# Kernel optimization log

Hardware: AMD Instinct MI355X
Metric: run time of the kernel (lower is better)

Reference implementation:

```python
import jax, jax.numpy as jnp
import numpy as np

NUM_RADII, NUM_THETA = 3, 16
RADIUS = 40.0
DT = 0.1
RELU_SHIFT = 0.2
B, N, NB, T_ENC, OTHER_CH = 4, 512, 512, 16, 3


def _rot_mats():
    # bin-center angles of the num_theta angular bins
    t = (jnp.arange(NUM_THETA, dtype=jnp.float32) + 0.5) * (2.0 * jnp.pi / NUM_THETA) - jnp.pi
    c, s = jnp.cos(t), jnp.sin(t)
    return jnp.stack([jnp.stack([c, -s], -1), jnp.stack([s, c], -1)], -2)  # [T,2,2]


def _steer_kernel(W):
    # W: [R,T,O,I,2,2]; equivariant steering K[r,t] = R(theta_t) W[r,t] R(theta_t)^T
    Rm = _rot_mats()
    K = jnp.einsum('tab,rtoibc,tdc->rtoiad', Rm, W, Rm)
    return K.reshape(NUM_RADII * NUM_THETA, W.shape[2], W.shape[3], 2, 2)  # [K,O,I,2,2]


def _equi_conv(src_pos, qry_pos, feats, mask, W):
    # src_pos [B,S,2], qry_pos [B,Q,2], feats [B,S,I,2] vector features, mask [B,Q,S]
    rel = src_pos[:, None, :, :] - qry_pos[:, :, None, :]          # [B,Q,S,2]
    d2 = jnp.sum(rel * rel, -1)
    dist = jnp.sqrt(d2 + 1e-9)
    theta = jnp.arctan2(rel[..., 1], rel[..., 0])
    rb = jnp.clip((dist / RADIUS * NUM_RADII).astype(jnp.int32), 0, NUM_RADII - 1)
    tb = jnp.mod(jnp.floor((theta + jnp.pi) / (2.0 * jnp.pi) * NUM_THETA).astype(jnp.int32), NUM_THETA)
    kidx = rb * NUM_THETA + tb                                     # [B,Q,S] polar bin id
    win = jnp.maximum(1.0 - d2 / (RADIUS * RADIUS), 0.0) ** 3      # smooth radial window
    w = win * mask
    H = jax.nn.one_hot(kidx, NUM_RADII * NUM_THETA, dtype=feats.dtype) * w[..., None]  # [B,Q,S,K]
    M = jnp.einsum('bqsk,bsiv->bqkiv', H, feats)                   # bin-accumulated neighbor features
    K = _steer_kernel(W)
    return jnp.einsum('bqkiv,koiuv->bqou', M, K)                   # [B,Q,O,2]


def _equi_linear(f, A, Bm):
    # rotation-equivariant linear on vector channels: (a*I + b*J) per (out,in)
    Jf = jnp.stack([-f[..., 1], f[..., 0]], -1)
    return jnp.einsum('oi,bniv->bnov', A, f) + jnp.einsum('oi,bniv->bnov', Bm, Jf)


def _forward(p0_enc, v0_enc, p0, v0, a, other_feats, box, box_feats, fluid_mask, box_mask,
             W_cf, W_co, A_df, B_df, layer_params):
    # update_pos_vel
    v1 = v0 + DT * a
    p1 = p0 + DT * (v0 + v1) * 0.5
    # forward(): feats = cat(other_feats, v0_enc) on channel dim -2
    feats = jnp.concatenate([other_feats, v0_enc], -2)
    # compute_correction
    fluid_feats = jnp.concatenate([v1[:, :, None, :], feats], -2)  # [B,N,20,2]
    out_conv_fluid = _equi_conv(p1, p1, fluid_feats, fluid_mask, W_cf)
    out_dense_fluid = _equi_linear(fluid_feats, A_df, B_df)
    out_conv_obst = _equi_conv(box, p1, box_feats[:, :, None, :], box_mask, W_co)
    output = jnp.concatenate([out_conv_obst, out_conv_fluid, out_dense_fluid], -2)  # [B,N,48,2]
    for (Wc, Ad, Bd) in layer_params:
        mags = (jnp.sum(output * output, -1) + 1e-6)[..., None]
        in_feats = output / mags * jax.nn.relu(mags - RELU_SHIFT)
        oc = _equi_conv(p1, p1, in_feats, fluid_mask, Wc)
        od = _equi_linear(in_feats, Ad, Bd)
        if od.shape[-2] == output.shape[-2]:
            output = oc + od + output
        else:
            output = oc + od
    corr = output / 128.0                                          # [B,N,1,2]
    # apply_correction
    p_corrected = p1 + corr[..., 0, :]
    v_corrected = (p_corrected - p0) / DT
    return p_corrected, v_corrected


def setup_inputs():
    key = jax.random.key(0)
    ks = jax.random.split(key, 32)
    d = {}
    d['p0_enc'] = jax.random.normal(ks[0], (B, N, T_ENC, 2), jnp.float32)
    d['v0_enc'] = jax.random.normal(ks[1], (B, N, T_ENC, 2), jnp.float32)
    d['p0'] = jax.random.uniform(ks[2], (B, N, 2), jnp.float32) * 100.0
    d['v0'] = jax.random.normal(ks[3], (B, N, 2), jnp.float32)
    d['a'] = jax.random.normal(ks[4], (B, N, 2), jnp.float32)
    d['other_feats'] = jax.random.normal(ks[5], (B, N, OTHER_CH, 2), jnp.float32)
    d['box'] = jax.random.uniform(ks[6], (B, NB, 2), jnp.float32) * 100.0
    d['box_feats'] = jax.random.normal(ks[7], (B, NB, 2), jnp.float32)
    d['fluid_mask'] = (jax.random.uniform(ks[8], (B, N, N)) < 0.5).astype(jnp.float32)
    d['box_mask'] = (jax.random.uniform(ks[9], (B, N, NB)) < 0.5).astype(jnp.float32)
    sc = 0.05
    d['W_cf'] = sc * jax.random.normal(ks[10], (NUM_RADII, NUM_THETA, 16, 20, 2, 2), jnp.float32)
    d['W_co'] = sc * jax.random.normal(ks[11], (NUM_RADII, NUM_THETA, 16, 1, 2, 2), jnp.float32)
    d['A_df'] = sc * jax.random.normal(ks[12], (16, 20), jnp.float32)
    d['B_df'] = sc * jax.random.normal(ks[13], (16, 20), jnp.float32)
    chans = [(32, 48), (32, 32), (32, 32), (1, 32)]
    for i, (o, ci) in enumerate(chans, start=1):
        d['W_c%d' % i] = sc * jax.random.normal(ks[13 + 3 * i], (NUM_RADII, NUM_THETA, o, ci, 2, 2), jnp.float32)
        d['A_d%d' % i] = sc * jax.random.normal(ks[14 + 3 * i], (o, ci), jnp.float32)
        d['B_d%d' % i] = sc * jax.random.normal(ks[15 + 3 * i], (o, ci), jnp.float32)
    return d


def reference(p0_enc, v0_enc, p0, v0, a, other_feats, box, box_feats, fluid_mask, box_mask,
              W_cf, W_co, A_df, B_df, W_c1, A_d1, B_d1, W_c2, A_d2, B_d2,
              W_c3, A_d3, B_d3, W_c4, A_d4, B_d4):
    layer_params = [(W_c1, A_d1, B_d1), (W_c2, A_d2, B_d2), (W_c3, A_d3, B_d3), (W_c4, A_d4, B_d4)]
    return _forward(p0_enc, v0_enc, p0, v0, a, other_feats, box, box_feats, fluid_mask, box_mask,
                    W_cf, W_co, A_df, B_df, layer_params)
```

## Files before the change

kernel.cpp:

```cpp
#include <hip/hip_runtime.h>
#include <cstdint>
#include <cstddef>

#define PI_F 3.14159265358979323846f

constexpr int BB = 4, NN = 512, BN = 2048, NBIN = 48;

typedef __attribute__((ext_vector_type(8))) short v8s;
typedef __attribute__((ext_vector_type(4))) float v4f;

__device__ __forceinline__ unsigned short f2bf(float f) {
  unsigned u = __float_as_uint(f);
  unsigned r = (u + 0x7FFFu + ((u >> 16) & 1u)) >> 16;
  return (unsigned short)r;
}
__device__ __forceinline__ float bf2f(unsigned short s) {
  return __uint_as_float(((unsigned)s) << 16);
}

__device__ __forceinline__ void steer_f32(const float* __restrict__ W, float* __restrict__ K2,
                                          int O, int I, int Ipad, int idx, int total) {
  if (idx >= total) return;
  int i = idx % Ipad;
  int o = (idx / Ipad) % O;
  int k = idx / (Ipad * O);
  int CTc = O * 2;
  size_t r0 = (size_t)((k*Ipad + i)*2 + 0) * CTc + o*2;
  size_t r1 = r0 + CTc;
  if (i >= I) { K2[r0]=0.f; K2[r0+1]=0.f; K2[r1]=0.f; K2[r1+1]=0.f; return; }
  int tt = k % 16;
  float ang = (tt + 0.5f) * (2.0f * PI_F / 16.0f) - PI_F;
  float ct = cosf(ang), st = sinf(ang);
  const float* Wp = W + ((size_t)(k*O + o)*I + i) * 4;
  float w00 = Wp[0], w01 = Wp[1], w10 = Wp[2], w11 = Wp[3];
  float rw00 = ct*w00 - st*w10, rw01 = ct*w01 - st*w11;
  float rw10 = st*w00 + ct*w10, rw11 = st*w01 + ct*w11;
  K2[r0 + 0] = rw00*ct - rw01*st;
  K2[r0 + 1] = rw10*ct - rw11*st;
  K2[r1 + 0] = rw00*st + rw01*ct;
  K2[r1 + 1] = rw10*st + rw11*ct;
}

__device__ __forceinline__ void steer_bf16T(const float* __restrict__ W,
                                            unsigned short* __restrict__ K2T,
                                            int O, int I, int Ipad, int Kd,
                                            int idx, int total) {
  if (idx >= total) return;
  int i = idx % Ipad;
  int o = (idx / Ipad) % O;
  int k = idx / (Ipad * O);
  size_t c0 = (size_t)(o*2 + 0) * Kd + (k*Ipad + i)*2;
  size_t c1 = (size_t)(o*2 + 1) * Kd + (k*Ipad + i)*2;
  if (i >= I) { K2T[c0]=0; K2T[c0+1]=0; K2T[c1]=0; K2T[c1+1]=0; return; }
  int tt = k % 16;
  float ang = (tt + 0.5f) * (2.0f * PI_F / 16.0f) - PI_F;
  float ct = cosf(ang), st = sinf(ang);
  const float* Wp = W + ((size_t)(k*O + o)*I + i) * 4;
  float w00 = Wp[0], w01 = Wp[1], w10 = Wp[2], w11 = Wp[3];
  float rw00 = ct*w00 - st*w10, rw01 = ct*w01 - st*w11;
  float rw10 = st*w00 + ct*w10, rw11 = st*w01 + ct*w11;
  K2T[c0 + 0] = f2bf(rw00*ct - rw01*st);
  K2T[c0 + 1] = f2bf(rw00*st + rw01*ct);
  K2T[c1 + 0] = f2bf(rw10*ct - rw11*st);
  K2T[c1 + 1] = f2bf(rw10*st + rw11*ct);
}

__global__ __launch_bounds__(256) void setup_kernel(
    const float* __restrict__ p0, const float* __restrict__ v0,
    const float* __restrict__ a, const float* __restrict__ other,
    const float* __restrict__ v0enc, float* __restrict__ p1, float* __restrict__ F0,
    const float* Wcf, unsigned short* K2CF, const float* Wco, float* K2CO,
    const float* Wc1, unsigned short* K2C1, const float* Wc2, unsigned short* K2C2,
    const float* Wc3, unsigned short* K2C3, const float* Wc4, float* K2C4) {
  int blk = blockIdx.x;
  int t = threadIdx.x;
  if (blk < 8) {
    int n = blk * 256 + t;
    float p0x = p0[n*2], p0y = p0[n*2+1];
    float v0x = v0[n*2], v0y = v0[n*2+1];
    float ax = a[n*2],  ay = a[n*2+1];
    float v1x = v0x + 0.1f*ax, v1y = v0y + 0.1f*ay;
    p1[n*2]   = p0x + 0.1f*(v0x+v1x)*0.5f;
    p1[n*2+1] = p0y + 0.1f*(v0y+v1y)*0.5f;
    float* F = F0 + (size_t)n*48;
    F[0] = v1x; F[1] = v1y;
    for (int c = 0; c < 3; ++c) {
      F[2+c*2]   = other[(n*3+c)*2];
      F[2+c*2+1] = other[(n*3+c)*2+1];
    }
    for (int c = 0; c < 16; ++c) {
      F[8+c*2]   = v0enc[(n*16+c)*2];
      F[8+c*2+1] = v0enc[(n*16+c)*2+1];
    }
    for (int c = 40; c < 48; ++c) F[c] = 0.0f;
  } else if (blk < 80)  steer_bf16T(Wcf, K2CF, 16, 20, 24, 2304, (blk-8)*256 + t, 18432);
  else if (blk < 83)  steer_f32(Wco, K2CO, 16, 1, 1,   (blk-80)*256 + t, 768);
  else if (blk < 371) steer_bf16T(Wc1, K2C1, 32, 48, 48, 4608, (blk-83)*256 + t, 73728);
  else if (blk < 563) steer_bf16T(Wc2, K2C2, 32, 32, 32, 3072, (blk-371)*256 + t, 49152);
  else if (blk < 755) steer_bf16T(Wc3, K2C3, 32, 32, 32, 3072, (blk-563)*256 + t, 49152);
  else                steer_f32(Wc4, K2C4, 1, 32, 32,  (blk-755)*256 + t, 1536);
}

__global__ __launch_bounds__(256) void pairs_all(const float* __restrict__ qry,
                                                 const float* __restrict__ srcF,
                                                 const float* __restrict__ maskF,
                                                 float* __restrict__ wlF, int* __restrict__ plF,
                                                 int* __restrict__ cntF,
                                                 const float* __restrict__ srcO,
                                                 const float* __restrict__ maskO,
                                                 float* __restrict__ wlO, int* __restrict__ plO,
                                                 int* __restrict__ cntO) {
  bool isBox = blockIdx.x >= 512;
  int qblk = isBox ? (blockIdx.x - 512) : blockIdx.x;
  const float* src = isBox ? srcO : srcF;
  const float* mask = isBox ? maskO : maskF;
  float* wlist = isBox ? wlO : wlF;
  int* plist = isBox ? plO : plF;
  int* cnt = isBox ? cntO : cntF;

  int wv = threadIdx.x >> 6;
  int lane = threadIdx.x & 63;
  int q = qblk * 4 + wv;
  int b = q >> 9;
  float qx = qry[q*2], qy = qry[q*2+1];
  const float* sb = src + b*1024;
  const float* mb = mask + (size_t)q*512;
  float* wl = wlist + (size_t)q*512;
  int* pl = plist + (size_t)q*512;
  int base = 0;
  for (int ch = 0; ch < 8; ++ch) {
    int s = ch*64 + lane;
    float sx = sb[s*2], sy = sb[s*2+1];
    float rx = sx - qx, ry = sy - qy;
    float d2 = rx*rx + ry*ry;
    float m = mb[s];
    float wi = fmaxf(1.0f - d2 / 1600.0f, 0.0f);
    float w = wi*wi*wi*m;
    bool pred = w > 0.0f;
    int k = 0;
    if (pred) {
      float dist = sqrtf(d2 + 1e-9f);
      float theta = atan2f(ry, rx);
      int rb = (int)(dist / 40.0f * 3.0f);
      rb = rb > 2 ? 2 : rb;
      float u = (theta + PI_F) / (2.0f * PI_F) * 16.0f;
      int tb = ((int)floorf(u)) & 15;
      k = rb*16 + tb;
    }
    unsigned long long msk = __ballot(pred);
    int before = __popcll(msk & ((1ull<<lane)-1ull));
    if (pred) {
      wl[base + before] = w;
      pl[base + before] = (s<<6) | k;
    }
    base += __popcll(msk);
  }
  if (lane == 0) cnt[q] = base;
}

template<int C2>
__device__ __forceinline__ void accum_loop(float* __restrict__ M, int sw, int c, int nnz,
    const float* __restrict__ wls, const int* __restrict__ pls,
    const float* __restrict__ fb) {
  if (nnz <= 0) return;
  constexpr int W = 16;
  float wA[W], fA[W]; int kA[W];
  #pragma unroll
  for (int j = 0; j < W; ++j) {
    bool v = j < nnz;
    float wv = v ? wls[j] : 0.0f;
    int p = v ? pls[j] : 0;
    wA[j] = wv; kA[j] = (p & 63) * C2;
    fA[j] = fb[(p >> 6) * C2];
  }
  for (int base = 0; base < nnz; base += W) {
    float wB[W], fB[W]; int kB[W];
    if (base + W < nnz) {
      #pragma unroll
      for (int j = 0; j < W; ++j) {
        int idx = base + W + j;
        bool v = idx < nnz;
        float wv = v ? wls[idx] : 0.0f;
        int p = v ? pls[idx] : 0;
        wB[j] = wv; kB[j] = (p & 63) * C2;
        fB[j] = fb[(p >> 6) * C2];
      }
    }
    #pragma unroll
    for (int j = 0; j < W; ++j) M[(kA[j] + c) ^ sw] += wA[j] * fA[j];
    #pragma unroll
    for (int j = 0; j < W; ++j) { wA[j] = wB[j]; kA[j] = kB[j]; fA[j] = fB[j]; }
  }
}

template<int QB, int TPB>
__device__ __forceinline__ void stage_lists(int q0, const int* __restrict__ csh,
    const float* __restrict__ wlist, const int* __restrict__ plist,
    float* __restrict__ wsh, int* __restrict__ psh) {
  const int t = threadIdx.x;
  for (int i = t; i < QB*128; i += TPB) {
    int qs = i >> 7, j = i & 127;
    if (j*4 < csh[qs]) {
      ((float4*)(wsh + qs*512))[j] = ((const float4*)(wlist + (size_t)(q0+qs)*512))[j];
      ((int4*)(psh + qs*512))[j]   = ((const int4*)(plist + (size_t)(q0+qs)*512))[j];
    }
  }
}

template<int C2, int QB, int TPB>
__global__ __launch_bounds__(TPB, 2) void accum4(const float* __restrict__ wlist,
                                                 const int* __restrict__ plist,
                                                 const int* __restrict__ cnt,
                                                 const float* __restrict__ feats,
                                                 unsigned short* __restrict__ Mout) {
  constexpr int Kd = NBIN * C2;
  static_assert(TPB == QB * C2, "TPB must equal QB*C2");
  __shared__ float Ml[QB * Kd];
  __shared__ float wsh[QB*512];
  __shared__ int   psh[QB*512];
  __shared__ int   csh[QB];
  const int t = threadIdx.x;
  const int q0 = blockIdx.x * QB;
  for (int i = t; i < QB*Kd; i += TPB) Ml[i] = 0.0f;
  if (t < QB) csh[t] = cnt[q0 + t];
  __syncthreads();
  stage_lists<QB, TPB>(q0, csh, wlist, plist, wsh, psh);
  __syncthreads();
  {
    const int ql = t / C2, c = t % C2;
    const int q = q0 + ql;
    accum_loop<C2>(Ml + ql*Kd, 0, c, csh[ql],
                   wsh + ql*512, psh + ql*512,
                   feats + (size_t)(q >> 9)*512*C2 + c);
  }
  __syncthreads();
  unsigned* dst = (unsigned*)(Mout + (size_t)q0 * Kd);
  const float2* s2 = (const float2*)Ml;
  for (int i = t; i < QB*(Kd/2); i += TPB) {
    float2 v = s2[i];
    dst[i] = (unsigned)f2bf(v.x) | ((unsigned)f2bf(v.y) << 16);
  }
}

template<int CT>
__global__ __launch_bounds__(256) void gemm_mfma(const unsigned short* __restrict__ A,
                                                 const unsigned short* __restrict__ B,
                                                 float* __restrict__ G, int Kd, int kn) {
  const int lane = threadIdx.x & 63;
  const int w = threadIdx.x >> 6;
  const int mblk = blockIdx.x;
  const int ks = blockIdx.y * 4 + w;
  const int k0 = ks * kn;
  const int m = lane & 15, quad = lane >> 4;
  constexpr int NT = CT / 16;
  const unsigned short* Ar0 = A + (size_t)(mblk*32 + m) * Kd + k0 + quad*8;
  const unsigned short* Ar1 = Ar0 + (size_t)16 * Kd;
  const unsigned short* Bp[NT];
  #pragma unroll
  for (int nt = 0; nt < NT; ++nt)
    Bp[nt] = B + (size_t)(nt*16 + m) * Kd + k0 + quad*8;
  v4f acc[2][NT];
  #pragma unroll
  for (int mt = 0; mt < 2; ++mt)
    for (int nt = 0; nt < NT; ++nt)
      acc[mt][nt] = (v4f){0.0f, 0.0f, 0.0f, 0.0f};
  for (int kt = 0; kt < kn; kt += 32) {
    v8s a0 = *(const v8s*)(Ar0 + kt);
    v8s a1 = *(const v8s*)(Ar1 + kt);
    #pragma unroll
    for (int nt = 0; nt < NT; ++nt) {
      v8s bv = *(const v8s*)(Bp[nt] + kt);
      acc[0][nt] = __builtin_amdgcn_mfma_f32_16x16x32_bf16(a0, bv, acc[0][nt], 0, 0, 0);
      acc[1][nt] = __builtin_amdgcn_mfma_f32_16x16x32_bf16(a1, bv, acc[1][nt], 0, 0, 0);
    }
  }
  float* Gb = G + ((size_t)ks * BN + mblk*32) * CT;
  #pragma unroll
  for (int mt = 0; mt < 2; ++mt)
    for (int nt = 0; nt < NT; ++nt)
      for (int r = 0; r < 4; ++r)
        Gb[(mt*16 + quad*4 + r) * CT + nt*16 + m] = acc[mt][nt][r];
}

__global__ void epilogueL(const float* __restrict__ Gp, int SPLIT,
                          const float* __restrict__ inPrev, int I,
                          const float* __restrict__ Ad, const float* __restrict__ Bd,
                          const float* __restrict__ prevOut, int doRes,
                          float* __restrict__ outCur, float* __restrict__ inNext) {
  int idx = blockIdx.x * blockDim.x + threadIdx.x;
  if (idx >= BN*32) return;
  int o = idx % 32, q = idx / 32;
  float x = 0.0f, y = 0.0f;
  for (int sp = 0; sp < SPLIT; ++sp) {
    size_t base = ((size_t)sp*BN + q)*64 + o*2;
    x += Gp[base]; y += Gp[base+1];
  }
  const float* f = inPrev + (size_t)q * I * 2;
  for (int i = 0; i < I; ++i) {
    float fx = f[i*2], fy = f[i*2+1];
    float Av = Ad[o*I+i], Bv = Bd[o*I+i];
    x += Av*fx - Bv*fy;
    y += Av*fy + Bv*fx;
  }
  if (doRes) {
    x += prevOut[(size_t)idx*2];
    y += prevOut[(size_t)idx*2+1];
  }
  outCur[(size_t)idx*2]   = x;
  outCur[(size_t)idx*2+1] = y;
  float m = x*x + y*y + 1e-6f;
  float sc = fmaxf(m - 0.2f, 0.0f) / m;
  inNext[(size_t)idx*2]   = x * sc;
  inNext[(size_t)idx*2+1] = y * sc;
}

__global__ __launch_bounds__(256) void fused_s0(
    const float* __restrict__ wlF, const int* __restrict__ plF, const int* __restrict__ cntF,
    const float* __restrict__ F0, const unsigned short* __restrict__ K2CF,
    const float* __restrict__ wlO, const int* __restrict__ plO, const int* __restrict__ cntO,
    const float* __restrict__ boxf, const float* __restrict__ K2CO,
    const float* __restrict__ Adf, const float* __restrict__ Bdf,
    float* __restrict__ in1) {
  constexpr int QB = 4;
  constexpr int Kd = 2304;
  constexpr int KW = 576;
  __shared__ float Ml[QB * Kd];
  __shared__ float Mo[QB * 96];
  __shared__ float red[4][QB * 32];
  __shared__ float wshF[QB*512];
  __shared__ int   pshF[QB*512];
  __shared__ float wshO[QB*512];
  __shared__ int   pshO[QB*512];
  __shared__ int cshF[QB];
  __shared__ int cshO[QB];
  const int t = threadIdx.x;
  const int q0 = blockIdx.x * QB;
  for (int i = t; i < QB*Kd; i += 256) Ml[i] = 0.0f;
  for (int i = t; i < QB*96; i += 256) Mo[i] = 0.0f;
  if (t < QB) cshF[t] = cntF[q0 + t];
  else if (t < 2*QB) cshO[t-QB] = cntO[q0 + t - QB];
  __syncthreads();
  for (int i = t; i < 2*QB*128; i += 256) {
    int half = i >> 9;
    int qs = (i >> 7) & (QB-1), j = i & 127;
    if (half == 0) {
      if (j*4 < cshF[qs]) {
        ((float4*)(wshF + qs*512))[j] = ((const float4*)(wlF + (size_t)(q0+qs)*512))[j];
        ((int4*)(pshF + qs*512))[j]   = ((const int4*)(plF + (size_t)(q0+qs)*512))[j];
      }
    } else {
      if (j*4 < cshO[qs]) {
        ((float4*)(wshO + qs*512))[j] = ((const float4*)(wlO + (size_t)(q0+qs)*512))[j];
        ((int4*)(pshO + qs*512))[j]   = ((const int4*)(plO + (size_t)(q0+qs)*512))[j];
      }
    }
  }
  __syncthreads();
  if (t < 192) {
    const int ql = t / 48, c = t % 48;
    const int q = q0 + ql;
    accum_loop<48>(Ml + ql*Kd, (ql & 3) << 2, c, cshF[ql],
                   wshF + ql*512, pshF + ql*512,
                   F0 + (size_t)(q >> 9)*512*48 + c);
  } else if (t < 200) {
    const int idx = t - 192;
    const int ql = idx >> 1, c = idx & 1;
    const int q = q0 + ql;
    accum_loop<2>(Mo + ql*96, 0, c, cshO[ql],
                  wshO + ql*512, pshO + ql*512,
                  boxf + (size_t)(q >> 9)*1024 + c);
  }
  __syncthreads();
  {
    const int lane = t & 63, w = t >> 6;
    const int m = lane & 15, quad = lane >> 4;
    const int ar = m & 3;
    const int sw = ar << 2;
    const float* Abase = Ml + ar * Kd;
    const int kb = w * KW + quad * 8;
    const unsigned short* Bb0 = K2CF + (size_t)m * Kd + kb;
    const unsigned short* Bb1 = K2CF + (size_t)(16 + m) * Kd + kb;
    v4f acc[2];
    acc[0] = (v4f){0,0,0,0}; acc[1] = (v4f){0,0,0,0};
    float4 a0c = *(const float4*)(Abase + (kb ^ sw));
    float4 a1c = *(const float4*)(Abase + ((kb + 4) ^ sw));
    v8s b0c = *(const v8s*)(Bb0);
    v8s b1c = *(const v8s*)(Bb1);
    for (int kt = 0; kt < KW; kt += 32) {
      float4 a0n, a1n; v8s b0n, b1n;
      if (kt + 32 < KW) {
        const int jn = kb + kt + 32;
        a0n = *(const float4*)(Abase + (jn ^ sw));
        a1n = *(const float4*)(Abase + ((jn + 4) ^ sw));
        b0n = *(const v8s*)(Bb0 + kt + 32);
        b1n = *(const v8s*)(Bb1 + kt + 32);
      }
      v8s av;
      av[0]=(short)f2bf(a0c.x); av[1]=(short)f2bf(a0c.y); av[2]=(short)f2bf(a0c.z); av[3]=(short)f2bf(a0c.w);
      av[4]=(short)f2bf(a1c.x); av[5]=(short)f2bf(a1c.y); av[6]=(short)f2bf(a1c.z); av[7]=(short)f2bf(a1c.w);
      acc[0] = __builtin_amdgcn_mfma_f32_16x16x32_bf16(av, b0c, acc[0], 0, 0, 0);
      acc[1] = __builtin_amdgcn_mfma_f32_16x16x32_bf16(av, b1c, acc[1], 0, 0, 0);
      a0c = a0n; a1c = a1n; b0c = b0n; b1c = b1n;
    }
    if (quad == 0) {
      #pragma unroll
      for (int nt = 0; nt < 2; ++nt)
        #pragma unroll
        for (int r = 0; r < 4; ++r)
          red[w][r*32 + nt*16 + m] = acc[nt][r];
    }
  }
  __syncthreads();
  if (t < 192) {
    const int ql = t / 48, ch = t % 48;
    const int q = q0 + ql;
    float x = 0.0f, y = 0.0f;
    if (ch < 16) {
      const float* Mq = Mo + ql*96;
      for (int j = 0; j < 96; ++j) {
        float mv = Mq[j];
        x += mv * K2CO[j*32 + ch*2];
        y += mv * K2CO[j*32 + ch*2 + 1];
      }
    } else if (ch < 32) {
      int o = ch - 16;
      x = red[0][ql*32+o*2] + red[1][ql*32+o*2] + red[2][ql*32+o*2] + red[3][ql*32+o*2];
      y = red[0][ql*32+o*2+1] + red[1][ql*32+o*2+1] + red[2][ql*32+o*2+1] + red[3][ql*32+o*2+1];
    } else {
      int o = ch - 32;
      const float* f = F0 + (size_t)q*48;
      for (int i = 0; i < 20; ++i) {
        float fx = f[i*2], fy = f[i*2+1];
        float Av = Adf[o*20+i], Bv = Bdf[o*20+i];
        x += Av*fx - Bv*fy;
        y += Av*fy + Bv*fx;
      }
    }
    float mm = x*x + y*y + 1e-6f;
    float sc = fmaxf(mm - 0.2f, 0.0f) / mm;
    size_t idx = (size_t)q*48 + ch;
    in1[idx*2]   = x * sc;
    in1[idx*2+1] = y * sc;
  }
}

template<int C2, int CT, int I, int QB>
__global__ __launch_bounds__(C2*QB) void fused_layer(
    const float* __restrict__ wlist, const int* __restrict__ plist,
    const int* __restrict__ cnt, const float* __restrict__ feats,
    const unsigned short* __restrict__ K2T,
    const float* __restrict__ Ad, const float* __restrict__ Bd,
    const float* __restrict__ prevOut, int doRes,
    float* __restrict__ outCur, float* __restrict__ inNext) {
  constexpr int Kd = NBIN * C2;
  constexpr int TPB = C2 * QB;
  constexpr int NW = TPB / 64;
  constexpr int KW = Kd / NW;
  constexpr int NT = CT / 16;
  static_assert(KW % 32 == 0, "KW must be multiple of 32");
  __shared__ float Ml[QB * Kd];
  __shared__ float red[NW][QB * CT];
  __shared__ float wsh[QB*512];
  __shared__ int   psh[QB*512];
  __shared__ int csh[QB];
  const int t = threadIdx.x;
  const int q0 = blockIdx.x * QB;
  for (int i = t; i < QB*Kd; i += TPB) Ml[i] = 0.0f;
  if (t < QB) csh[t] = cnt[q0 + t];
  __syncthreads();
  stage_lists<QB, TPB>(q0, csh, wlist, plist, wsh, psh);
  __syncthreads();
  {
    const int ql = t / C2, c = t % C2;
    const int q = q0 + ql;
    accum_loop<C2>(Ml + ql*Kd, (ql & 3) << 2, c, csh[ql],
                   wsh + ql*512, psh + ql*512,
                   feats + (size_t)(q >> 9)*512*C2 + c);
  }
  __syncthreads();
  const int lane = t & 63, w = t >> 6;
  const int m = lane & 15, quad = lane >> 4;
  const int ar = m & (QB-1);
  const int sw = ar << 2;
  const float* Abase = Ml + ar * Kd;
  const int kb = w * KW + quad * 8;
  const unsigned short* Bb[NT];
  #pragma unroll
  for (int nt = 0; nt < NT; ++nt)
    Bb[nt] = K2T + (size_t)(nt*16 + m) * Kd + kb;
  v4f acc[NT];
  #pragma unroll
  for (int nt = 0; nt < NT; ++nt) acc[nt] = (v4f){0,0,0,0};
  float4 a0c = *(const float4*)(Abase + (kb ^ sw));
  float4 a1c = *(const float4*)(Abase + ((kb + 4) ^ sw));
  v8s bc[NT];
  #pragma unroll
  for (int nt = 0; nt < NT; ++nt) bc[nt] = *(const v8s*)(Bb[nt]);
  for (int kt = 0; kt < KW; kt += 32) {
    float4 a0n, a1n; v8s bn[NT];
    if (kt + 32 < KW) {
      const int jn = kb + kt + 32;
      a0n = *(const float4*)(Abase + (jn ^ sw));
      a1n = *(const float4*)(Abase + ((jn + 4) ^ sw));
      #pragma unroll
      for (int nt = 0; nt < NT; ++nt) bn[nt] = *(const v8s*)(Bb[nt] + kt + 32);
    }
    v8s av;
    av[0]=(short)f2bf(a0c.x); av[1]=(short)f2bf(a0c.y); av[2]=(short)f2bf(a0c.z); av[3]=(short)f2bf(a0c.w);
    av[4]=(short)f2bf(a1c.x); av[5]=(short)f2bf(a1c.y); av[6]=(short)f2bf(a1c.z); av[7]=(short)f2bf(a1c.w);
    #pragma unroll
    for (int nt = 0; nt < NT; ++nt)
      acc[nt] = __builtin_amdgcn_mfma_f32_16x16x32_bf16(av, bc[nt], acc[nt], 0, 0, 0);
    a0c = a0n; a1c = a1n;
    #pragma unroll
    for (int nt = 0; nt < NT; ++nt) bc[nt] = bn[nt];
  }
  if (quad == 0) {
    #pragma unroll
    for (int nt = 0; nt < NT; ++nt)
      #pragma unroll
      for (int r = 0; r < QB; ++r)
        red[w][r*CT + nt*16 + m] = acc[nt][r];
  }
  __syncthreads();
  if (t < QB * (CT/2)) {
    const int o = t % (CT/2), ql = t / (CT/2);
    const int q = q0 + ql;
    float x = 0.0f, y = 0.0f;
    #pragma unroll
    for (int w2 = 0; w2 < NW; ++w2) {
      x += red[w2][ql*CT + o*2];
      y += red[w2][ql*CT + o*2 + 1];
    }
    const float* f = feats + (size_t)q * C2;
    for (int i = 0; i < I; ++i) {
      float fx = f[i*2], fy = f[i*2+1];
      float Av = Ad[o*I + i], Bv = Bd[o*I + i];
      x += Av*fx - Bv*fy;
      y += Av*fy + Bv*fx;
    }
    size_t idx = (size_t)q * (CT/2) + o;
    if (doRes) { x += prevOut[idx*2]; y += prevOut[idx*2+1]; }
    outCur[idx*2]   = x;
    outCur[idx*2+1] = y;
    float mm = x*x + y*y + 1e-6f;
    float sc = fmaxf(mm - 0.2f, 0.0f) / mm;
    inNext[idx*2]   = x * sc;
    inNext[idx*2+1] = y * sc;
  }
}

__global__ __launch_bounds__(256) void fused_l4(
    const float* __restrict__ wl, const int* __restrict__ pl, const int* __restrict__ cnt,
    const float* __restrict__ in4, const float* __restrict__ K2C4,
    const float* __restrict__ Ad4, const float* __restrict__ Bd4,
    const float* __restrict__ p1, const float* __restrict__ p0,
    float* __restrict__ dout) {
  constexpr int QB = 4, Kd = 3072;
  __shared__ float Ml[QB * Kd];
  __shared__ float wsh[QB*512];
  __shared__ int   psh[QB*512];
  __shared__ int csh[QB];
  const int t = threadIdx.x;
  const int q0 = blockIdx.x * QB;
  for (int i = t; i < QB*Kd; i += 256) Ml[i] = 0.0f;
  if (t < QB) csh[t] = cnt[q0 + t];
  __syncthreads();
  stage_lists<QB, 256>(q0, csh, wl, pl, wsh, psh);
  __syncthreads();
  {
    const int ql = t / 64, c = t % 64;
    const int q = q0 + ql;
    accum_loop<64>(Ml + ql*Kd, (ql & 3) << 2, c, csh[ql],
                   wsh + ql*512, psh + ql*512,
                   in4 + (size_t)(q >> 9)*512*64 + c);
  }
  __syncthreads();
  const int lane = t & 63, w = t >> 6;
  const int q = q0 + w;
  const int sw = (w & 3) << 2;
  const float* Mq = Ml + w*Kd;
  float a0 = 0.0f, a1 = 0.0f;
  for (int j = lane; j < Kd; j += 64) {
    float av = Mq[j ^ sw];
    a0 += av * K2C4[j*2];
    a1 += av * K2C4[j*2+1];
  }
  if (lane < 32) {
    float fx = in4[q*64 + lane*2], fy = in4[q*64 + lane*2 + 1];
    float Av = Ad4[lane], Bv = Bd4[lane];
    a0 += Av*fx - Bv*fy;
    a1 += Av*fy + Bv*fx;
  }
  for (int off = 32; off > 0; off >>= 1) {
    a0 += __shfl_down(a0, off);
    a1 += __shfl_down(a1, off);
  }
  if (lane == 0) {
    float px = p1[q*2]   + a0/128.0f;
    float py = p1[q*2+1] + a1/128.0f;
    dout[q*2] = px; dout[q*2+1] = py;
    dout[4096 + q*2]   = (px - p0[q*2]) / 0.1f;
    dout[4096 + q*2+1] = (py - p0[q*2+1]) / 0.1f;
  }
}

extern "C" void kernel_launch(void* const* d_in, const int* in_sizes, int n_in,
                              void* d_out, int out_size, void* d_ws, size_t ws_size,
                              hipStream_t stream) {
  (void)in_sizes; (void)n_in; (void)out_size; (void)ws_size;
  const float* v0_enc = (const float*)d_in[1];
  const float* p0     = (const float*)d_in[2];
  const float* v0     = (const float*)d_in[3];
  const float* a      = (const float*)d_in[4];
  const float* other  = (const float*)d_in[5];
  const float* box    = (const float*)d_in[6];
  const float* boxf   = (const float*)d_in[7];
  const float* fmask  = (const float*)d_in[8];
  const float* bmask  = (const float*)d_in[9];
  const float* Wcf = (const float*)d_in[10];
  const float* Wco = (const float*)d_in[11];
  const float* Adf = (const float*)d_in[12];
  const float* Bdf = (const float*)d_in[13];
  const float* Wc1 = (const float*)d_in[14];
  const float* Ad1 = (const float*)d_in[15];
  const float* Bd1 = (const float*)d_in[16];
  const float* Wc2 = (const float*)d_in[17];
  const float* Ad2 = (const float*)d_in[18];
  const float* Bd2 = (const float*)d_in[19];
  const float* Wc3 = (const float*)d_in[20];
  const float* Ad3 = (const float*)d_in[21];
  const float* Bd3 = (const float*)d_in[22];
  const float* Wc4 = (const float*)d_in[23];
  const float* Ad4 = (const float*)d_in[24];
  const float* Bd4 = (const float*)d_in[25];

  float* ws = (float*)d_ws;
  float* P1    = ws + 0;
  float* F0    = ws + 4096;
  unsigned short* K2CF = (unsigned short*)(ws + 102400);
  float* K2CO  = ws + 176128;
  unsigned short* K2C1 = (unsigned short*)(ws + 179200);
  unsigned short* K2C2 = (unsigned short*)(ws + 474112);
  unsigned short* K2C3 = (unsigned short*)(ws + 670720);
  float* K2C4  = ws + 867328;
  float* WFl   = ws + 873472;
  int*   PFl   = (int*)(ws + 1922048);
  int*   CNTF  = (int*)(ws + 2970624);
  int*   CNTO  = (int*)(ws + 2972672);
  float* IN1   = ws + 2974720;
  float* IN2   = ws + 3171328;
  float* IN3   = ws + 3302400;
  float* IN4   = ws + 3433472;
  float* OUTA  = ws + 3564544;
  float* OUTB  = ws + 3695616;
  float* GPART = ws + 4027392;
  unsigned short* MBUF = (unsigned short*)(ws + 6124544);
  float* WOl   = ws + 15561728;
  int*   POl   = (int*)(ws + 16610304);

  setup_kernel<<<761, 256, 0, stream>>>(p0, v0, a, other, v0_enc, P1, F0,
                                        Wcf, K2CF, Wco, K2CO, Wc1, K2C1,
                                        Wc2, K2C2, Wc3, K2C3, Wc4, K2C4);
  pairs_all<<<1024, 256, 0, stream>>>(P1, P1, fmask, WFl, PFl, CNTF,
                                      box, bmask, WOl, POl, CNTO);
  fused_s0<<<512, 256, 0, stream>>>(WFl, PFl, CNTF, F0, K2CF,
                                    WOl, POl, CNTO, boxf, K2CO, Adf, Bdf, IN1);
  accum4<96, 2, 192><<<1024, 192, 0, stream>>>(WFl, PFl, CNTF, IN1, MBUF);
  gemm_mfma<64><<<dim3(64, 4), 256, 0, stream>>>(MBUF, K2C1, GPART, 4608, 288);
  epilogueL<<<256, 256, 0, stream>>>(GPART, 16, IN1, 48, Ad1, Bd1, nullptr, 0, OUTA, IN2);
  fused_layer<64, 64, 32, 4><<<512, 256, 0, stream>>>(WFl, PFl, CNTF, IN2, K2C2,
                                                      Ad2, Bd2, OUTA, 1, OUTB, IN3);
  fused_layer<64, 64, 32, 4><<<512, 256, 0, stream>>>(WFl, PFl, CNTF, IN3, K2C3,
                                                      Ad3, Bd3, OUTB, 1, OUTA, IN4);
  fused_l4<<<512, 256, 0, stream>>>(WFl, PFl, CNTF, IN4, K2C4, Ad4, Bd4,
                                    P1, p0, (float*)d_out);
}
```

Baseline: 321.6 us.

## Split fused layers 2-3 into separate accumulate, GEMM and epilogue kernels

Layers 2 and 3 no longer use the fused per-block accumulate+MFMA kernel. Each now runs the same three-stage path as layer 1: accum4 writes the binned features as bf16 to a global buffer, a split-K MFMA GEMM follows, then an epilogue kernel. accum4 gains bounds guards so QB=3 blocks work on 2048 queries. The aim is better GEMM efficiency and occupancy, at the cost of a global round trip of the M matrix and extra kernel launches.

```diff
diff --git a/kernel.cpp b/kernel.cpp
--- a/kernel.cpp
+++ b/kernel.cpp
@@ -222,7 +222,7 @@
   const int t = threadIdx.x;
   const int q0 = blockIdx.x * QB;
   for (int i = t; i < QB*Kd; i += TPB) Ml[i] = 0.0f;
-  if (t < QB) csh[t] = cnt[q0 + t];
+  if (t < QB) csh[t] = (q0 + t < BN) ? cnt[q0 + t] : 0;
   __syncthreads();
   stage_lists<QB, TPB>(q0, csh, wlist, plist, wsh, psh);
   __syncthreads();
@@ -234,9 +234,11 @@
                    feats + (size_t)(q >> 9)*512*C2 + c);
   }
   __syncthreads();
+  const int rows = (q0 + QB <= BN) ? QB : (BN - q0);
   unsigned* dst = (unsigned*)(Mout + (size_t)q0 * Kd);
   const float2* s2 = (const float2*)Ml;
-  for (int i = t; i < QB*(Kd/2); i += TPB) {
+  const int lim = rows * (Kd/2);
+  for (int i = t; i < lim; i += TPB) {
     float2 v = s2[i];
     dst[i] = (unsigned)f2bf(v.x) | ((unsigned)f2bf(v.y) << 16);
   }
@@ -444,112 +446,6 @@
   }
 }
 
-template<int C2, int CT, int I, int QB>
-__global__ __launch_bounds__(C2*QB) void fused_layer(
-    const float* __restrict__ wlist, const int* __restrict__ plist,
-    const int* __restrict__ cnt, const float* __restrict__ feats,
-    const unsigned short* __restrict__ K2T,
-    const float* __restrict__ Ad, const float* __restrict__ Bd,
-    const float* __restrict__ prevOut, int doRes,
-    float* __restrict__ outCur, float* __restrict__ inNext) {
-  constexpr int Kd = NBIN * C2;
-  constexpr int TPB = C2 * QB;
-  constexpr int NW = TPB / 64;
-  constexpr int KW = Kd / NW;
-  constexpr int NT = CT / 16;
-  static_assert(KW % 32 == 0, "KW must be multiple of 32");
-  __shared__ float Ml[QB * Kd];
-  __shared__ float red[NW][QB * CT];
-  __shared__ float wsh[QB*512];
-  __shared__ int   psh[QB*512];
-  __shared__ int csh[QB];
-  const int t = threadIdx.x;
-  const int q0 = blockIdx.x * QB;
-  for (int i = t; i < QB*Kd; i += TPB) Ml[i] = 0.0f;
-  if (t < QB) csh[t] = cnt[q0 + t];
-  __syncthreads();
-  stage_lists<QB, TPB>(q0, csh, wlist, plist, wsh, psh);
-  __syncthreads();
-  {
-    const int ql = t / C2, c = t % C2;
-    const int q = q0 + ql;
-    accum_loop<C2>(Ml + ql*Kd, (ql & 3) << 2, c, csh[ql],
-                   wsh + ql*512, psh + ql*512,
-                   feats + (size_t)(q >> 9)*512*C2 + c);
-  }
-  __syncthreads();
-  const int lane = t & 63, w = t >> 6;
-  const int m = lane & 15, quad = lane >> 4;
-  const int ar = m & (QB-1);
-  const int sw = ar << 2;
-  const float* Abase = Ml + ar * Kd;
-  const int kb = w * KW + quad * 8;
-  const unsigned short* Bb[NT];
-  #pragma unroll
-  for (int nt = 0; nt < NT; ++nt)
-    Bb[nt] = K2T + (size_t)(nt*16 + m) * Kd + kb;
-  v4f acc[NT];
-  #pragma unroll
-  for (int nt = 0; nt < NT; ++nt) acc[nt] = (v4f){0,0,0,0};
-  float4 a0c = *(const float4*)(Abase + (kb ^ sw));
-  float4 a1c = *(const float4*)(Abase + ((kb + 4) ^ sw));
-  v8s bc[NT];
-  #pragma unroll
-  for (int nt = 0; nt < NT; ++nt) bc[nt] = *(const v8s*)(Bb[nt]);
-  for (int kt = 0; kt < KW; kt += 32) {
-    float4 a0n, a1n; v8s bn[NT];
-    if (kt + 32 < KW) {
-      const int jn = kb + kt + 32;
-      a0n = *(const float4*)(Abase + (jn ^ sw));
-      a1n = *(const float4*)(Abase + ((jn + 4) ^ sw));
-      #pragma unroll
-      for (int nt = 0; nt < NT; ++nt) bn[nt] = *(const v8s*)(Bb[nt] + kt + 32);
-    }
-    v8s av;
-    av[0]=(short)f2bf(a0c.x); av[1]=(short)f2bf(a0c.y); av[2]=(short)f2bf(a0c.z); av[3]=(short)f2bf(a0c.w);
-    av[4]=(short)f2bf(a1c.x); av[5]=(short)f2bf(a1c.y); av[6]=(short)f2bf(a1c.z); av[7]=(short)f2bf(a1c.w);
-    #pragma unroll
-    for (int nt = 0; nt < NT; ++nt)
-      acc[nt] = __builtin_amdgcn_mfma_f32_16x16x32_bf16(av, bc[nt], acc[nt], 0, 0, 0);
-    a0c = a0n; a1c = a1n;
-    #pragma unroll
-    for (int nt = 0; nt < NT; ++nt) bc[nt] = bn[nt];
-  }
-  if (quad == 0) {
-    #pragma unroll
-    for (int nt = 0; nt < NT; ++nt)
-      #pragma unroll
-      for (int r = 0; r < QB; ++r)
-        red[w][r*CT + nt*16 + m] = acc[nt][r];
-  }
-  __syncthreads();
-  if (t < QB * (CT/2)) {
-    const int o = t % (CT/2), ql = t / (CT/2);
-    const int q = q0 + ql;
-    float x = 0.0f, y = 0.0f;
-    #pragma unroll
-    for (int w2 = 0; w2 < NW; ++w2) {
-      x += red[w2][ql*CT + o*2];
-      y += red[w2][ql*CT + o*2 + 1];
-    }
-    const float* f = feats + (size_t)q * C2;
-    for (int i = 0; i < I; ++i) {
-      float fx = f[i*2], fy = f[i*2+1];
-      float Av = Ad[o*I + i], Bv = Bd[o*I + i];
-      x += Av*fx - Bv*fy;
-      y += Av*fy + Bv*fx;
-    }
-    size_t idx = (size_t)q * (CT/2) + o;
-    if (doRes) { x += prevOut[idx*2]; y += prevOut[idx*2+1]; }
-    outCur[idx*2]   = x;
-    outCur[idx*2+1] = y;
-    float mm = x*x + y*y + 1e-6f;
-    float sc = fmaxf(mm - 0.2f, 0.0f) / mm;
-    inNext[idx*2]   = x * sc;
-    inNext[idx*2+1] = y * sc;
-  }
-}
-
 __global__ __launch_bounds__(256) void fused_l4(
     const float* __restrict__ wl, const int* __restrict__ pl, const int* __restrict__ cnt,
     const float* __restrict__ in4, const float* __restrict__ K2C4,
@@ -669,10 +565,12 @@
   accum4<96, 2, 192><<<1024, 192, 0, stream>>>(WFl, PFl, CNTF, IN1, MBUF);
   gemm_mfma<64><<<dim3(64, 4), 256, 0, stream>>>(MBUF, K2C1, GPART, 4608, 288);
   epilogueL<<<256, 256, 0, stream>>>(GPART, 16, IN1, 48, Ad1, Bd1, nullptr, 0, OUTA, IN2);
-  fused_layer<64, 64, 32, 4><<<512, 256, 0, stream>>>(WFl, PFl, CNTF, IN2, K2C2,
-                                                      Ad2, Bd2, OUTA, 1, OUTB, IN3);
-  fused_layer<64, 64, 32, 4><<<512, 256, 0, stream>>>(WFl, PFl, CNTF, IN3, K2C3,
-                                                      Ad3, Bd3, OUTB, 1, OUTA, IN4);
+  accum4<64, 3, 192><<<683, 192, 0, stream>>>(WFl, PFl, CNTF, IN2, MBUF);
+  gemm_mfma<64><<<dim3(64, 4), 256, 0, stream>>>(MBUF, K2C2, GPART, 3072, 192);
+  epilogueL<<<256, 256, 0, stream>>>(GPART, 16, IN2, 32, Ad2, Bd2, OUTA, 1, OUTB, IN3);
+  accum4<64, 3, 192><<<683, 192, 0, stream>>>(WFl, PFl, CNTF, IN3, MBUF);
+  gemm_mfma<64><<<dim3(64, 4), 256, 0, stream>>>(MBUF, K2C3, GPART, 3072, 192);
+  epilogueL<<<256, 256, 0, stream>>>(GPART, 16, IN3, 32, Ad3, Bd3, OUTB, 1, OUTA, IN4);
   fused_l4<<<512, 256, 0, stream>>>(WFl, PFl, CNTF, IN4, K2C4, Ad4, Bd4,
                                     P1, p0, (float*)d_out);
 }
```

Result: slower. 332.4 us (+3.4%).
